# Kernel tuning notes

Hardware: AMD Instinct MI355X
Metric: run time of the kernel (lower is better)

## Reference

```python
import jax, jax.numpy as jnp
import numpy as np

N = 100000
E = 1600000
F_IN = 256
H1, C1 = 4, 32          # layer 1: heads=4, out_channels=32, concat=True -> 128
H2, C2 = 1, 16          # layer 2: heads=1, out_channels=nclass=16, concat=False
SLOPE = 0.2             # leaky relu negative slope


def setup_inputs() -> dict:
    key = jax.random.key(0)
    ks = jax.random.split(key, 10)
    x = jax.random.normal(ks[0], (N, F_IN), dtype=jnp.float32)
    row = jax.random.randint(ks[1], (E,), 0, N, dtype=jnp.int32)      # source j
    off = jax.random.randint(ks[2], (E,), 1, N, dtype=jnp.int32)
    col = ((row + off) % N).astype(jnp.int32)                          # target i, no self loops
    edge_index = jnp.stack([row, col])

    def glorot(k, shape, fan_in, fan_out):
        lim = np.sqrt(6.0 / (fan_in + fan_out))
        return jax.random.uniform(k, shape, jnp.float32, -lim, lim)

    W1 = glorot(ks[3], (F_IN, H1 * C1), F_IN, H1 * C1)
    att1 = glorot(ks[4], (1, H1, 2 * C1), H1, 2 * C1)
    b1 = jnp.zeros((H1 * C1,), jnp.float32)
    W2 = glorot(ks[5], (H1 * C1, H2 * C2), H1 * C1, H2 * C2)
    att2 = glorot(ks[6], (1, H2, 2 * C2), H2, 2 * C2)
    b2 = jnp.zeros((C2,), jnp.float32)
    return {"x": x, "edge_index": edge_index, "W1": W1, "att1": att1,
            "b1": b1, "W2": W2, "att2": att2, "b2": b2}


def gcn_norm(edge_index, num_nodes):
    # add_remaining_self_loops + symmetric normalization (GeoLayer.norm)
    loop = jnp.arange(num_nodes, dtype=edge_index.dtype)
    row = jnp.concatenate([edge_index[0], loop])
    col = jnp.concatenate([edge_index[1], loop])
    w = jnp.ones(row.shape[0], jnp.float32)
    deg = jax.ops.segment_sum(w, row, num_segments=num_nodes)
    dinv = jnp.where(deg > 0, jax.lax.rsqrt(deg), 0.0)
    return row, col, dinv[row] * w * dinv[col]


def segment_softmax(alpha, seg, num_segments):
    amax = jax.ops.segment_max(alpha, seg, num_segments=num_segments)
    ex = jnp.exp(alpha - amax[seg])
    denom = jax.ops.segment_sum(ex, seg, num_segments=num_segments)
    return ex / (denom[seg] + 1e-16)


def geo_layer(x, row, col, ew, W, att, b, heads, out_ch, concat):
    n = x.shape[0]
    xt = (x @ W).reshape(n, heads, out_ch)
    x_i = xt[col]                         # [E+N, H, C] target features
    x_j = xt[row]                         # [E+N, H, C] source features
    wl, wr = att[:, :, :out_ch], att[:, :, out_ch:]
    # (cat([x_i,x_j],-1) * att).sum(-1) == (x_i*wl).sum + (x_j*wr).sum
    alpha = (x_i * wl).sum(-1) + (x_j * wr).sum(-1)     # [E+N, H]
    alpha = jnp.where(alpha >= 0, alpha, SLOPE * alpha)  # leaky_relu
    alpha = segment_softmax(alpha, col, n)
    msg = ew[:, None, None] * x_j * alpha[:, :, None]    # [E+N, H, C]
    out = jax.ops.segment_sum(msg, col, num_segments=n)  # scatter-add to targets
    out = out.reshape(n, heads * out_ch) if concat else out.mean(axis=1)
    return out + b


def reference(x, edge_index, W1, att1, b1, W2, att2, b2):
    # norm is identical for both layers (edge_weight=None each time)
    row, col, ew = gcn_norm(edge_index, x.shape[0])
    h = geo_layer(x, row, col, ew, W1, att1, b1, H1, C1, True)
    h = jax.nn.relu(h)
    out = geo_layer(h, row, col, ew, W2, att2, b2, H2, C2, False)
    return out
```

## Files before the change

### kernel.cpp

```cpp
#include <hip/hip_runtime.h>
#include <math.h>

#define TPB 256
#define SEGN 512
#define SCAP 14336
#define CHB 8192
#define CAPC 12288

__device__ __forceinline__ float lrelu(float a){ return a >= 0.f ? a : 0.2f*a; }

typedef __attribute__((ext_vector_type(8))) short bf16x8;
typedef __attribute__((ext_vector_type(4))) float f32x4;

__device__ __forceinline__ unsigned short bfr(float f){
  unsigned u = __float_as_uint(f);
  return (unsigned short)((u + 0x7fffu + ((u >> 16) & 1u)) >> 16);
}

__device__ __forceinline__ void gl_lds16(const void* g, void* l){
  __builtin_amdgcn_global_load_lds(
      (const __attribute__((address_space(1))) void*)g,
      (__attribute__((address_space(3))) void*)l, 16, 0, 0);
}


__global__ void k_binit(int* __restrict__ bcurC, int* __restrict__ bcurR, int NSEG2){
  int t = threadIdx.x;
  if(t < NSEG2){ bcurC[t] = t*CAPC; bcurR[t] = t*CAPC; }
}

__global__ __launch_bounds__(256) void k_bucket2(const int* __restrict__ rows, const int* __restrict__ cols,
    int* __restrict__ bcurC, int* __restrict__ bcurR,
    unsigned* __restrict__ ebufC, unsigned short* __restrict__ ebufR, int E, int NSEG2){
  __shared__ int lhist[256];
  __shared__ int lbase[256];
  int tid = threadIdx.x;
  int e0 = blockIdx.x * CHB;
  #pragma unroll 1
  for(int r=0; r<4; r++){
    lhist[tid] = 0;
    __syncthreads();
    int eb = e0 + r*2048;
    unsigned pk[8]; int sg[8], rk[8];
    #pragma unroll
    for(int i=0;i<8;i++){
      int e = eb + i*256 + tid;
      sg[i] = -1;
      if(e < E){
        int cc = cols[e], rr = rows[e];
        sg[i] = cc >> 9;
        pk[i] = ((unsigned)(cc & (SEGN-1)) << 17) | (unsigned)rr;
        rk[i] = atomicAdd(&lhist[sg[i]], 1);
      }
    }
    __syncthreads();
    if(tid < NSEG2){
      int c = lhist[tid];
      lbase[tid] = c ? atomicAdd(&bcurC[tid], c) : 0;
    }
    __syncthreads();
    #pragma unroll
    for(int i=0;i<8;i++)
      if(sg[i] >= 0){
        int p = lbase[sg[i]] + rk[i];
        if(p < (sg[i]+1)*CAPC) ebufC[p] = pk[i];
      }
    __syncthreads();
  }
  #pragma unroll 1
  for(int r=0; r<4; r++){
    lhist[tid] = 0;
    __syncthreads();
    int eb = e0 + r*2048;
    int sg[8], rk[8]; unsigned short pv[8];
    #pragma unroll
    for(int i=0;i<8;i++){
      int e = eb + i*256 + tid;
      sg[i] = -1;
      if(e < E){
        int rr = rows[e];
        sg[i] = rr >> 9;
        pv[i] = (unsigned short)(rr & (SEGN-1));
        rk[i] = atomicAdd(&lhist[sg[i]], 1);
      }
    }
    __syncthreads();
    if(tid < NSEG2){
      int c = lhist[tid];
      lbase[tid] = c ? atomicAdd(&bcurR[tid], c) : 0;
    }
    __syncthreads();
    #pragma unroll
    for(int i=0;i<8;i++)
      if(sg[i] >= 0){
        int p = lbase[sg[i]] + rk[i];
        if(p < (sg[i]+1)*CAPC) ebufR[p] = pv[i];
      }
    __syncthreads();
  }
}

__global__ __launch_bounds__(256) void k_cntseg(const int* __restrict__ bcurC, const int* __restrict__ bcurR,
    const unsigned* __restrict__ ebufC, const unsigned short* __restrict__ ebufR,
    int* __restrict__ cnt, float* __restrict__ dinv, int N){
  __shared__ int hc[SEGN];
  __shared__ int hr[SEGN];
  int s = blockIdx.x, tid = threadIdx.x;
  int lo = s*SEGN;
  int nn = min(SEGN, N - lo);
  for(int i=tid; i<SEGN; i+=256){ hc[i] = 0; hr[i] = 0; }
  __syncthreads();
  int cb = s*CAPC;
  int cc = min(bcurC[s] - cb, CAPC);
  int rc = min(bcurR[s] - cb, CAPC);
  for(int j=tid; j<cc; j+=256) atomicAdd(&hc[ebufC[cb + j] >> 17], 1);
  for(int j=tid; j<rc; j+=256) atomicAdd(&hr[ebufR[cb + j]], 1);
  __syncthreads();
  for(int i=tid; i<nn; i+=256){
    cnt[lo+i]  = hc[i] + 1;
    dinv[lo+i] = 1.f / sqrtf((float)(hr[i] + 1));
  }
}

__global__ void k_scan_block(const int* __restrict__ cnt, int* __restrict__ bsum, int N){
  __shared__ int sdata[256];
  int base = blockIdx.x*1024 + threadIdx.x*4;
  int s = 0;
  #pragma unroll
  for(int i=0;i<4;i++){ int idx = base+i; if(idx < N) s += cnt[idx]; }
  sdata[threadIdx.x] = s; __syncthreads();
  for(int off=128; off>0; off>>=1){
    if(threadIdx.x < off) sdata[threadIdx.x] += sdata[threadIdx.x+off];
    __syncthreads();
  }
  if(threadIdx.x == 0) bsum[blockIdx.x] = sdata[0];
}

__global__ void k_scan_bsum(int* bsum, int NB){
  __shared__ int s[256];
  int t = threadIdx.x;
  int v = (t < NB) ? bsum[t] : 0;
  s[t] = v; __syncthreads();
  for(int off=1; off<256; off<<=1){
    int add = (t >= off) ? s[t-off] : 0;
    __syncthreads();
    s[t] += add;
    __syncthreads();
  }
  if(t < NB) bsum[t] = s[t] - v;
}

__global__ void k_scan_write(const int* __restrict__ cnt, const int* __restrict__ bsum,
                             int* __restrict__ offs, int N){
  __shared__ int sdata[256];
  int t = threadIdx.x;
  int base = blockIdx.x*1024 + t*4;
  int v[4]; int s = 0;
  #pragma unroll
  for(int i=0;i<4;i++){ int idx = base+i; v[i] = (idx < N) ? cnt[idx] : 0; s += v[i]; }
  sdata[t] = s; __syncthreads();
  int mine = s;
  for(int off=1; off<256; off<<=1){
    int add = (t >= off) ? sdata[t-off] : 0;
    __syncthreads();
    sdata[t] += add;
    __syncthreads();
  }
  int run = sdata[t] - mine + bsum[blockIdx.x];
  #pragma unroll
  for(int i=0;i<4;i++){
    int idx = base+i;
    if(idx < N){
      offs[idx] = run;
      run += v[i];
      if(idx == N-1) offs[N] = run;
    }
  }
}

__global__ __launch_bounds__(256) void k_sortfill(const int* __restrict__ offs,
    const int* __restrict__ bcurC, const unsigned* __restrict__ ebuf,
    int* __restrict__ csr, int N){
  __shared__ int lcur[SEGN];
  __shared__ int lbuf[SCAP];
  int s = blockIdx.x, tid = threadIdx.x;
  int lo = s*SEGN;
  int nn = min(SEGN, N - lo);
  int base = offs[lo];
  int total = offs[lo+nn] - base;
  int eb = s*CAPC;
  int ec = min(bcurC[s] - eb, CAPC);
  if(total <= SCAP){
    for(int li=tid; li<nn; li+=256){
      int o = offs[lo+li] - base;
      lbuf[o]  = lo + li;
      lcur[li] = o + 1;
    }
    __syncthreads();
    for(int j=tid; j<ec; j+=256){
      unsigned pk = ebuf[eb + j];
      int li  = pk >> 17;
      int row = pk & 0x1FFFF;
      int p = atomicAdd(&lcur[li], 1);
      lbuf[p] = row;
    }
    __syncthreads();
    for(int j=tid; j<total; j+=256) csr[base + j] = lbuf[j];
  } else {
    for(int li=tid; li<nn; li+=256){
      int o = offs[lo+li];
      csr[o] = lo + li;
      lcur[li] = o + 1;
    }
    __syncthreads();
    for(int j=tid; j<ec; j+=256){
      unsigned pk = ebuf[eb + j];
      int li  = pk >> 17;
      int row = pk & 0x1FFFF;
      int p = atomicAdd(&lcur[li], 1);
      csr[p] = row;
    }
  }
}


__global__ void k_prepW(const float* __restrict__ W, short* __restrict__ Whi,
                        short* __restrict__ Wlo){
  int idx = blockIdx.x*256 + threadIdx.x;
  int n = idx >> 8, k = idx & 255;
  float f = W[k*128 + n];
  unsigned short h = bfr(f);
  float hf = __uint_as_float(((unsigned)h) << 16);
  Whi[n*256 + k] = (short)h;
  Wlo[n*256 + k] = (short)bfr(f - hf);
}


__global__ __launch_bounds__(256) void k_prepX(const float* __restrict__ x,
    unsigned short* __restrict__ xhi, unsigned short* __restrict__ xlo,
    long long Ntot, long long NtotPad){
  long long i = ((long long)blockIdx.x*256 + threadIdx.x)*8;
  if(i >= NtotPad) return;
  float v[8] = {0.f,0.f,0.f,0.f,0.f,0.f,0.f,0.f};
  if(i < Ntot){
    const float4* x4 = (const float4*)x;
    float4 a = x4[i>>2], b = x4[(i>>2)+1];
    v[0]=a.x; v[1]=a.y; v[2]=a.z; v[3]=a.w;
    v[4]=b.x; v[5]=b.y; v[6]=b.z; v[7]=b.w;
  }
  unsigned hp[4], lp[4];
  #pragma unroll
  for(int j=0;j<4;j++){
    unsigned short h0 = bfr(v[2*j]), h1 = bfr(v[2*j+1]);
    float r0 = v[2*j]   - __uint_as_float(((unsigned)h0)<<16);
    float r1 = v[2*j+1] - __uint_as_float(((unsigned)h1)<<16);
    hp[j] = (unsigned)h0 | ((unsigned)h1<<16);
    lp[j] = (unsigned)bfr(r0) | ((unsigned)bfr(r1)<<16);
  }
  *((uint4*)(xhi + i)) = make_uint4(hp[0],hp[1],hp[2],hp[3]);
  *((uint4*)(xlo + i)) = make_uint4(lp[0],lp[1],lp[2],lp[3]);
}


#define BUFB 24576
__global__ __launch_bounds__(256) void k_gemm1(
    const unsigned short* __restrict__ xhi, const unsigned short* __restrict__ xlo,
    const short* __restrict__ Whi, const short* __restrict__ Wlo,
    const float* __restrict__ att1,
    unsigned* __restrict__ xtb, float* __restrict__ sl, float* __restrict__ sr, int N){
  __shared__ __align__(16) char smem[2*BUFB];
  float* fx = (float*)smem;
  float* att_sh = (float*)(smem + 17408);

  int tid = threadIdx.x;
  int n0 = blockIdx.x * 64;
  int w = tid >> 6, l = tid & 63;
  int wm = w & 1, wn = w >> 1;
  int lm = l & 15, lq = l >> 4;

  f32x4 acc[2][4];
  #pragma unroll
  for(int a=0;a<2;a++)
    #pragma unroll
    for(int b=0;b<4;b++) acc[a][b] = (f32x4){0.f,0.f,0.f,0.f};

  int ua = (w<<6) | l;
  int ar = ua >> 2, aq = ua & 3;
  int as_ = aq ^ ((ar >> 1) & 3);
  const unsigned short* gAh = xhi + (size_t)(n0 + ar)*256 + as_*8;
  const unsigned short* gAl = xlo + (size_t)(n0 + ar)*256 + as_*8;
  int ub0 = (w<<6) | l,  ub1 = 256 + ub0;
  int br0 = ub0 >> 2, bs0 = (ub0 & 3) ^ ((br0 >> 1) & 3);
  int br1 = ub1 >> 2, bs1 = (ub1 & 3) ^ ((br1 >> 1) & 3);
  const short* gBh0 = Whi + br0*256 + bs0*8;
  const short* gBh1 = Whi + br1*256 + bs1*8;
  const short* gBl0 = Wlo + br0*256 + bs0*8;
  const short* gBl1 = Wlo + br1*256 + bs1*8;
  int woff = w << 10;

  int offA[2], offB[4];
  #pragma unroll
  for(int mt=0;mt<2;mt++){
    int rr = wm*32 + mt*16 + lm;
    offA[mt] = rr*32 + ((lq ^ ((rr>>1)&3)) << 3);
  }
  #pragma unroll
  for(int nt=0;nt<4;nt++){
    int rr = wn*64 + nt*16 + lm;
    offB[nt] = rr*32 + ((lq ^ ((rr>>1)&3)) << 3);
  }

  {
    char* base = smem;
    gl_lds16(gAh,  base          + woff);
    gl_lds16(gAl,  base + 4096   + woff);
    gl_lds16(gBh0, base + 8192   + woff);
    gl_lds16(gBh1, base + 12288  + woff);
    gl_lds16(gBl0, base + 16384  + woff);
    gl_lds16(gBl1, base + 20480  + woff);
  }
  __syncthreads();

  int cur = 0;
  #pragma unroll 1
  for(int c=0;c<8;c++){
    if(c < 7){
      int kb = (c+1) << 5;
      char* base = smem + (cur^1)*BUFB;
      gl_lds16(gAh  + kb, base          + woff);
      gl_lds16(gAl  + kb, base + 4096   + woff);
      gl_lds16(gBh0 + kb, base + 8192   + woff);
      gl_lds16(gBh1 + kb, base + 12288  + woff);
      gl_lds16(gBl0 + kb, base + 16384  + woff);
      gl_lds16(gBl1 + kb, base + 20480  + woff);
    }
    short* Ah = (short*)(smem + cur*BUFB);
    short* Al = (short*)(smem + cur*BUFB + 4096);
    short* Bh = (short*)(smem + cur*BUFB + 8192);
    short* Bl = (short*)(smem + cur*BUFB + 16384);
    bf16x8 ah[2], al2[2];
    #pragma unroll
    for(int mt=0;mt<2;mt++){
      ah[mt]  = *((bf16x8*)&Ah[offA[mt]]);
      al2[mt] = *((bf16x8*)&Al[offA[mt]]);
    }
    #pragma unroll
    for(int nt=0;nt<4;nt++){
      bf16x8 bh = *((bf16x8*)&Bh[offB[nt]]);
      bf16x8 bl = *((bf16x8*)&Bl[offB[nt]]);
      #pragma unroll
      for(int mt=0;mt<2;mt++){
        acc[mt][nt] = __builtin_amdgcn_mfma_f32_16x16x32_bf16(ah[mt],  bh, acc[mt][nt], 0,0,0);
        acc[mt][nt] = __builtin_amdgcn_mfma_f32_16x16x32_bf16(ah[mt],  bl, acc[mt][nt], 0,0,0);
        acc[mt][nt] = __builtin_amdgcn_mfma_f32_16x16x32_bf16(al2[mt], bh, acc[mt][nt], 0,0,0);
      }
    }
    __syncthreads();
    cur ^= 1;
  }

  #pragma unroll
  for(int mt=0;mt<2;mt++){
    #pragma unroll
    for(int v=0;v<4;v++){
      int row = n0 + wm*32 + mt*16 + lq*4 + v;
      if(row < N){
        unsigned p0 = (unsigned)bfr(acc[mt][0][v]) | ((unsigned)bfr(acc[mt][2][v])<<16);
        unsigned p1 = (unsigned)bfr(acc[mt][1][v]) | ((unsigned)bfr(acc[mt][3][v])<<16);
        int jb = wn*32 + lm;
        xtb[(size_t)row*64 + jb]      = p0;
        xtb[(size_t)row*64 + jb + 16] = p1;
      }
    }
  }

  att_sh[tid] = att1[tid];
  #pragma unroll 1
  for(int p=0;p<2;p++){
    __syncthreads();
    if(wn == p){
      #pragma unroll
      for(int mt=0;mt<2;mt++)
        #pragma unroll
        for(int nt=0;nt<4;nt++)
          #pragma unroll
          for(int v=0;v<4;v++)
            fx[(wm*32 + mt*16 + lq*4 + v)*68 + nt*16 + lm] = acc[mt][nt][v];
    }
    __syncthreads();
    if(tid < 128){
      int rloc = tid >> 1, hh = tid & 1;
      int head = p*2 + hh;
      float a = 0.f, b = 0.f;
      #pragma unroll
      for(int c4=0;c4<8;c4++){
        float4 xv  = *((const float4*)&fx[rloc*68 + hh*32 + c4*4]);
        float4 alv = *((const float4*)&att_sh[head*64 + c4*4]);
        float4 arv = *((const float4*)&att_sh[head*64 + 32 + c4*4]);
        a += xv.x*alv.x + xv.y*alv.y + xv.z*alv.z + xv.w*alv.w;
        b += xv.x*arv.x + xv.y*arv.y + xv.z*arv.z + xv.w*arv.w;
      }
      int row = n0 + rloc;
      if(row < N){
        sl[(size_t)row*4 + head] = a;
        sr[(size_t)row*4 + head] = b;
      }
    }
  }
}


__global__ __launch_bounds__(64) void k_agg1(const int* __restrict__ offs, const int* __restrict__ srcs,
    const float* __restrict__ sl, const float* __restrict__ sr, const float* __restrict__ dinv,
    const unsigned* __restrict__ xtb, const float* __restrict__ b1, float* __restrict__ h, int N){
  __shared__ int   s_sh[64];
  __shared__ float w_sh[64*4];
  int n = blockIdx.x;
  if(n >= N) return;
  int lane = threadIdx.x;
  int beg = offs[n], end = offs[n+1];
  int deg = end - beg;
  float4 sln = *((const float4*)(sl + (size_t)n*4));
  int h0 = lane >> 5;
  float den0=0.f,den1=0.f,den2=0.f,den3=0.f;
  float acc0=0.f, acc1=0.f;

  if(deg <= 64){
    int j = beg + lane;
    int s = 0; float wd = 0.f;
    float a0=-1e30f, a1=-1e30f, a2=-1e30f, a3=-1e30f;
    if(j < end){
      s = srcs[j];
      float4 a = *((const float4*)(sr + (size_t)s*4));
      a0 = lrelu(sln.x + a.x);
      a1 = lrelu(sln.y + a.y);
      a2 = lrelu(sln.z + a.z);
      a3 = lrelu(sln.w + a.w);
      wd = dinv[s];
    }
    float m0=a0,m1=a1,m2=a2,m3=a3;
    #pragma unroll
    for(int o=32;o>0;o>>=1){
      m0 = fmaxf(m0, __shfl_xor(m0,o));
      m1 = fmaxf(m1, __shfl_xor(m1,o));
      m2 = fmaxf(m2, __shfl_xor(m2,o));
      m3 = fmaxf(m3, __shfl_xor(m3,o));
    }
    den0 = __expf(a0 - m0);
    den1 = __expf(a1 - m1);
    den2 = __expf(a2 - m2);
    den3 = __expf(a3 - m3);
    s_sh[lane] = s;
    w_sh[lane*4+0] = wd*den0;
    w_sh[lane*4+1] = wd*den1;
    w_sh[lane*4+2] = wd*den2;
    w_sh[lane*4+3] = wd*den3;
    __syncthreads();
    int k = 0;
    for(; k+8<=deg; k+=8){
      int sk[8];
      #pragma unroll
      for(int u=0;u<8;u++) sk[u] = __builtin_amdgcn_readfirstlane(s_sh[k+u]);
      unsigned pv[8];
      #pragma unroll
      for(int u=0;u<8;u++) pv[u] = xtb[(size_t)sk[u]*64 + lane];
      #pragma unroll
      for(int u=0;u<8;u++){
        float2 wv = *((const float2*)&w_sh[(k+u)*4 + h0*2]);
        acc0 += wv.x * __uint_as_float(pv[u] << 16);
        acc1 += wv.y * __uint_as_float(pv[u] & 0xffff0000u);
      }
    }
    for(; k<deg; k++){
      int sk = __builtin_amdgcn_readfirstlane(s_sh[k]);
      unsigned pvv = xtb[(size_t)sk*64 + lane];
      float2 wv = *((const float2*)&w_sh[k*4 + h0*2]);
      acc0 += wv.x * __uint_as_float(pvv << 16);
      acc1 += wv.y * __uint_as_float(pvv & 0xffff0000u);
    }
  } else {
    float m0=-1e30f,m1=-1e30f,m2=-1e30f,m3=-1e30f;
    for(int j=beg+lane; j<end; j+=64){
      int s = srcs[j];
      float4 a = *((const float4*)(sr + (size_t)s*4));
      m0 = fmaxf(m0, lrelu(sln.x + a.x));
      m1 = fmaxf(m1, lrelu(sln.y + a.y));
      m2 = fmaxf(m2, lrelu(sln.z + a.z));
      m3 = fmaxf(m3, lrelu(sln.w + a.w));
    }
    #pragma unroll
    for(int o=32;o>0;o>>=1){
      m0 = fmaxf(m0, __shfl_xor(m0,o));
      m1 = fmaxf(m1, __shfl_xor(m1,o));
      m2 = fmaxf(m2, __shfl_xor(m2,o));
      m3 = fmaxf(m3, __shfl_xor(m3,o));
    }
    for(int c0=beg; c0<end; c0+=64){
      int cnt = min(64, end-c0);
      int j = c0 + lane;
      float e0=0.f,e1=0.f,e2=0.f,e3=0.f, wd=0.f; int s=0;
      if(j<end){
        s = srcs[j];
        float4 a = *((const float4*)(sr + (size_t)s*4));
        e0 = __expf(lrelu(sln.x + a.x) - m0);
        e1 = __expf(lrelu(sln.y + a.y) - m1);
        e2 = __expf(lrelu(sln.z + a.z) - m2);
        e3 = __expf(lrelu(sln.w + a.w) - m3);
        wd = dinv[s];
      }
      den0+=e0; den1+=e1; den2+=e2; den3+=e3;
      s_sh[lane] = s;
      w_sh[lane*4+0] = wd*e0;
      w_sh[lane*4+1] = wd*e1;
      w_sh[lane*4+2] = wd*e2;
      w_sh[lane*4+3] = wd*e3;
      __syncthreads();
      int k = 0;
      for(; k+8<=cnt; k+=8){
        int sk[8];
        #pragma unroll
        for(int u=0;u<8;u++) sk[u] = __builtin_amdgcn_readfirstlane(s_sh[k+u]);
        unsigned pv[8];
        #pragma unroll
        for(int u=0;u<8;u++) pv[u] = xtb[(size_t)sk[u]*64 + lane];
        #pragma unroll
        for(int u=0;u<8;u++){
          float2 wv = *((const float2*)&w_sh[(k+u)*4 + h0*2]);
          acc0 += wv.x * __uint_as_float(pv[u] << 16);
          acc1 += wv.y * __uint_as_float(pv[u] & 0xffff0000u);
        }
      }
      for(; k<cnt; k++){
        int sk = __builtin_amdgcn_readfirstlane(s_sh[k]);
        unsigned pvv = xtb[(size_t)sk*64 + lane];
        float2 wv = *((const float2*)&w_sh[k*4 + h0*2]);
        acc0 += wv.x * __uint_as_float(pvv << 16);
        acc1 += wv.y * __uint_as_float(pvv & 0xffff0000u);
      }
      __syncthreads();
    }
  }
  #pragma unroll
  for(int o=32;o>0;o>>=1){
    den0 += __shfl_xor(den0,o);
    den1 += __shfl_xor(den1,o);
    den2 += __shfl_xor(den2,o);
    den3 += __shfl_xor(den3,o);
  }
  float din = dinv[n];
  int ch0 = (lane < 32) ? lane : lane + 32;
  int ch1 = ch0 + 32;
  float d0 = (lane < 32) ? den0 : den2;
  float d1 = (lane < 32) ? den1 : den3;
  float o0 = din*acc0/(d0 + 1e-16f) + b1[ch0];
  float o1 = din*acc1/(d1 + 1e-16f) + b1[ch1];
  h[(size_t)n*128 + ch0] = o0 > 0.f ? o0 : 0.f;
  h[(size_t)n*128 + ch1] = o1 > 0.f ? o1 : 0.f;
}


__global__ __launch_bounds__(256) void k_gemm2(const float* __restrict__ hmat, const float* __restrict__ W2,
    const float* __restrict__ att2, unsigned* __restrict__ xt2b,
    float* __restrict__ sl2, float* __restrict__ sr2, int N){
  __shared__ float hs[16*132];
  __shared__ float ws[16*132];
  __shared__ float xs[16*16];
  int t = threadIdx.x;
  int n0 = blockIdx.x * 16;
  #pragma unroll
  for(int i=0;i<8;i++){
    int idx = t + 256*i;
    int k = idx >> 4, c = idx & 15;
    ws[c*132 + k] = W2[idx];
  }
  #pragma unroll
  for(int i=0;i<2;i++){
    int idx = t + 256*i;
    int r = idx >> 5, k4 = idx & 31;
    int n = n0 + r;
    float4 v = make_float4(0.f,0.f,0.f,0.f);
    if(n < N) v = ((const float4*)hmat)[(size_t)n*32 + k4];
    *((float4*)&hs[r*132 + k4*4]) = v;
  }
  __syncthreads();
  int r = t >> 4, c = t & 15;
  float acc = 0.f;
  for(int k=0;k<128;k+=4){
    float4 hv = *((const float4*)&hs[r*132+k]);
    float4 wv = *((const float4*)&ws[c*132+k]);
    acc += hv.x*wv.x + hv.y*wv.y + hv.z*wv.z + hv.w*wv.w;
  }
  xs[r*16 + c] = acc;
  __syncthreads();
  int n = n0 + r;
  if(c < 8 && n < N){
    unsigned pk = (unsigned)bfr(xs[r*16+c]) | ((unsigned)bfr(xs[r*16+c+8])<<16);
    xt2b[(size_t)n*8 + c] = pk;
  }
  if(t < 16){
    int nn = n0 + t;
    if(nn < N){
      float a = 0.f, b = 0.f;
      #pragma unroll
      for(int cc=0;cc<16;cc++){ float v = xs[t*16+cc]; a += v*att2[cc]; b += v*att2[16+cc]; }
      sl2[nn] = a; sr2[nn] = b;
    }
  }
}


__global__ __launch_bounds__(64) void k_agg2(const int* __restrict__ offs, const int* __restrict__ srcs,
    const float* __restrict__ sl2, const float* __restrict__ sr2, const float* __restrict__ dinv,
    const unsigned* __restrict__ xt2b, const float* __restrict__ b2, float* __restrict__ out, int N){
  __shared__ int   s_sh[64];
  __shared__ float w_sh[64];
  int n = blockIdx.x;
  if(n >= N) return;
  int lane = threadIdx.x;
  int beg = offs[n], end = offs[n+1];
  int deg = end - beg;
  float sln = sl2[n];
  float den = 0.f, acc0 = 0.f, acc1 = 0.f;
  int grp = lane >> 3, ch = lane & 7;

  if(deg <= 64){
    int j = beg + lane;
    int s = 0; float wd = 0.f; float a = -1e30f;
    if(j < end){
      s = srcs[j];
      a = lrelu(sln + sr2[s]);
      wd = dinv[s];
    }
    float m = a;
    #pragma unroll
    for(int o=32;o>0;o>>=1) m = fmaxf(m, __shfl_xor(m,o));
    float e = __expf(a - m);
    den = e;
    s_sh[lane] = s;
    w_sh[lane] = wd*e;
    __syncthreads();
    for(int k=0;k<deg;k+=8){
      int kk = k + grp;
      if(kk < deg){
        int sk = s_sh[kk];
        float wk = w_sh[kk];
        unsigned pv = xt2b[(size_t)sk*8 + ch];
        acc0 += wk * __uint_as_float(pv << 16);
        acc1 += wk * __uint_as_float(pv & 0xffff0000u);
      }
    }
  } else {
    float m = -1e30f;
    for(int j=beg+lane; j<end; j+=64)
      m = fmaxf(m, lrelu(sln + sr2[srcs[j]]));
    #pragma unroll
    for(int o=32;o>0;o>>=1) m = fmaxf(m, __shfl_xor(m,o));
    for(int c0=beg; c0<end; c0+=64){
      int cnt = min(64, end-c0);
      int j = c0 + lane;
      float e=0.f, wd=0.f; int s=0;
      if(j<end){
        s = srcs[j];
        e = __expf(lrelu(sln + sr2[s]) - m);
        wd = dinv[s];
      }
      den += e;
      s_sh[lane] = s;
      w_sh[lane] = wd*e;
      __syncthreads();
      for(int k=0;k<cnt;k+=8){
        int kk = k + grp;
        if(kk < cnt){
          int sk = s_sh[kk];
          float wk = w_sh[kk];
          unsigned pv = xt2b[(size_t)sk*8 + ch];
          acc0 += wk * __uint_as_float(pv << 16);
          acc1 += wk * __uint_as_float(pv & 0xffff0000u);
        }
      }
      __syncthreads();
    }
  }
  #pragma unroll
  for(int o=32;o>0;o>>=1) den += __shfl_xor(den,o);
  acc0 += __shfl_xor(acc0,8);  acc0 += __shfl_xor(acc0,16);  acc0 += __shfl_xor(acc0,32);
  acc1 += __shfl_xor(acc1,8);  acc1 += __shfl_xor(acc1,16);  acc1 += __shfl_xor(acc1,32);
  if(lane < 8){
    float din = dinv[n];
    out[(size_t)n*16 + lane]     = din*acc0/(den + 1e-16f) + b2[lane];
    out[(size_t)n*16 + lane + 8] = din*acc1/(den + 1e-16f) + b2[lane+8];
  }
}


extern "C" void kernel_launch(void* const* d_in, const int* in_sizes, int n_in,
                              void* d_out, int out_size, void* d_ws, size_t ws_size,
                              hipStream_t stream){
  const float* x    = (const float*)d_in[0];
  const int*   ei   = (const int*)d_in[1];
  const float* W1   = (const float*)d_in[2];
  const float* att1 = (const float*)d_in[3];
  const float* b1   = (const float*)d_in[4];
  const float* W2   = (const float*)d_in[5];
  const float* att2 = (const float*)d_in[6];
  const float* b2   = (const float*)d_in[7];
  int N = in_sizes[0] / 256;
  int E = in_sizes[1] / 2;
  const int* rows = ei;
  const int* cols = ei + E;
  float* out = (float*)d_out;

  int ET    = E + N;
  int Npad  = (N + 63) & ~63;
  int NSEG2 = (N + SEGN - 1) / SEGN;

  char* p = (char*)d_ws;
  auto alloc = [&](size_t bytes)->void*{ void* q = p; p += (bytes + 255) & ~(size_t)255; return q; };
  int*      cnt     = (int*)alloc((size_t)N*4);
  int*      offs    = (int*)alloc((size_t)(N+1)*4);
  int*      bsum    = (int*)alloc(256*4);
  int*      bcurC   = (int*)alloc(256*4);
  int*      bcurR   = (int*)alloc(256*4);
  int*      csr     = (int*)alloc((size_t)ET*4);
  float*    dinv    = (float*)alloc((size_t)N*4);
  unsigned* xtb     = (unsigned*)alloc((size_t)N*64*4);
  float*    sl1     = (float*)alloc((size_t)N*16);
  float*    sr1     = (float*)alloc((size_t)N*16);
  float*    hbuf    = (float*)alloc((size_t)Npad*512);
  unsigned* xt2b    = (unsigned*)alloc((size_t)N*8*4);
  float*    sl2     = (float*)alloc((size_t)N*4);
  float*    sr2     = (float*)alloc((size_t)N*4);
  short*    Whi     = (short*)alloc((size_t)128*256*2);
  short*    Wlo     = (short*)alloc((size_t)128*256*2);
  unsigned short* xhi = (unsigned short*)alloc((size_t)Npad*256*2);

  unsigned*       ebufC = (unsigned*)xtb;
  unsigned short* ebufR = (unsigned short*)(ebufC + (size_t)NSEG2*CAPC);
  unsigned short* xlo   = (unsigned short*)hbuf;

  int NB = (N + 1023) / 1024;
  int gB = (E + CHB - 1) / CHB;

  k_binit<<<1, 256, 0, stream>>>(bcurC, bcurR, NSEG2);
  k_bucket2<<<gB, 256, 0, stream>>>(rows, cols, bcurC, bcurR, ebufC, ebufR, E, NSEG2);
  k_cntseg<<<NSEG2, 256, 0, stream>>>(bcurC, bcurR, ebufC, ebufR, cnt, dinv, N);
  k_scan_block<<<NB, 256, 0, stream>>>(cnt, bsum, N);
  k_scan_bsum<<<1, 256, 0, stream>>>(bsum, NB);
  k_scan_write<<<NB, 256, 0, stream>>>(cnt, bsum, offs, N);
  k_sortfill<<<NSEG2, 256, 0, stream>>>(offs, bcurC, ebufC, csr, N);

  k_prepW<<<128, 256, 0, stream>>>(W1, Whi, Wlo);
  long long Ntot = (long long)N*256, NtotPad = (long long)Npad*256;
  k_prepX<<<(int)((NtotPad + 2047)/2048), 256, 0, stream>>>(x, xhi, xlo, Ntot, NtotPad);
  k_gemm1<<<(N + 63)/64, 256, 0, stream>>>(xhi, xlo, Whi, Wlo, att1, xtb, sl1, sr1, N);
  k_agg1<<<N, 64, 0, stream>>>(offs, csr, sl1, sr1, dinv, xtb, b1, hbuf, N);

  k_gemm2<<<(N + 15)/16, 256, 0, stream>>>(hbuf, W2, att2, xt2b, sl2, sr2, N);
  k_agg2<<<N, 64, 0, stream>>>(offs, csr, sl2, sr2, dinv, xt2b, b2, out, N);
}
```

Measured before the change: 447.4 us.

## Fuse bf16 split of x into GEMM1 and merge scan stages into count kernel

```diff
diff --git a/kernel.cpp b/kernel.cpp
--- a/kernel.cpp
+++ b/kernel.cpp
@@ -23,11 +23,6 @@
       (__attribute__((address_space(3))) void*)l, 16, 0, 0);
 }
 
-
-__global__ void k_binit(int* __restrict__ bcurC, int* __restrict__ bcurR, int NSEG2){
-  int t = threadIdx.x;
-  if(t < NSEG2){ bcurC[t] = t*CAPC; bcurR[t] = t*CAPC; }
-}
 
 __global__ __launch_bounds__(256) void k_bucket2(const int* __restrict__ rows, const int* __restrict__ cols,
     int* __restrict__ bcurC, int* __restrict__ bcurR,
@@ -63,7 +58,7 @@
     for(int i=0;i<8;i++)
       if(sg[i] >= 0){
         int p = lbase[sg[i]] + rk[i];
-        if(p < (sg[i]+1)*CAPC) ebufC[p] = pk[i];
+        if(p < CAPC) ebufC[sg[i]*CAPC + p] = pk[i];
       }
     __syncthreads();
   }
@@ -94,7 +89,7 @@
     for(int i=0;i<8;i++)
       if(sg[i] >= 0){
         int p = lbase[sg[i]] + rk[i];
-        if(p < (sg[i]+1)*CAPC) ebufR[p] = pv[i];
+        if(p < CAPC) ebufR[sg[i]*CAPC + p] = pv[i];
       }
     __syncthreads();
   }
@@ -102,38 +97,34 @@
 
 __global__ __launch_bounds__(256) void k_cntseg(const int* __restrict__ bcurC, const int* __restrict__ bcurR,
     const unsigned* __restrict__ ebufC, const unsigned short* __restrict__ ebufR,
-    int* __restrict__ cnt, float* __restrict__ dinv, int N){
+    int* __restrict__ cnt, float* __restrict__ dinv, int* __restrict__ bsum, int N){
   __shared__ int hc[SEGN];
   __shared__ int hr[SEGN];
+  __shared__ int red[256];
   int s = blockIdx.x, tid = threadIdx.x;
   int lo = s*SEGN;
   int nn = min(SEGN, N - lo);
   for(int i=tid; i<SEGN; i+=256){ hc[i] = 0; hr[i] = 0; }
   __syncthreads();
   int cb = s*CAPC;
-  int cc = min(bcurC[s] - cb, CAPC);
-  int rc = min(bcurR[s] - cb, CAPC);
+  int cc = min(bcurC[s], CAPC);
+  int rc = min(bcurR[s], CAPC);
   for(int j=tid; j<cc; j+=256) atomicAdd(&hc[ebufC[cb + j] >> 17], 1);
   for(int j=tid; j<rc; j+=256) atomicAdd(&hr[ebufR[cb + j]], 1);
   __syncthreads();
+  int tsum = 0;
   for(int i=tid; i<nn; i+=256){
-    cnt[lo+i]  = hc[i] + 1;
+    int c = hc[i] + 1;
+    cnt[lo+i]  = c;
+    tsum += c;
     dinv[lo+i] = 1.f / sqrtf((float)(hr[i] + 1));
   }
-}
-
-__global__ void k_scan_block(const int* __restrict__ cnt, int* __restrict__ bsum, int N){
-  __shared__ int sdata[256];
-  int base = blockIdx.x*1024 + threadIdx.x*4;
-  int s = 0;
-  #pragma unroll
-  for(int i=0;i<4;i++){ int idx = base+i; if(idx < N) s += cnt[idx]; }
-  sdata[threadIdx.x] = s; __syncthreads();
+  red[tid] = tsum; __syncthreads();
   for(int off=128; off>0; off>>=1){
-    if(threadIdx.x < off) sdata[threadIdx.x] += sdata[threadIdx.x+off];
-    __syncthreads();
-  }
-  if(threadIdx.x == 0) bsum[blockIdx.x] = sdata[0];
+    if(tid < off) red[tid] += red[tid+off];
+    __syncthreads();
+  }
+  if(tid == 0) bsum[s] = red[0];
 }
 
 __global__ void k_scan_bsum(int* bsum, int NB){
@@ -154,10 +145,10 @@
                              int* __restrict__ offs, int N){
   __shared__ int sdata[256];
   int t = threadIdx.x;
-  int base = blockIdx.x*1024 + t*4;
-  int v[4]; int s = 0;
-  #pragma unroll
-  for(int i=0;i<4;i++){ int idx = base+i; v[i] = (idx < N) ? cnt[idx] : 0; s += v[i]; }
+  int base = blockIdx.x*512 + t*2;
+  int v0 = (base   < N) ? cnt[base]   : 0;
+  int v1 = (base+1 < N) ? cnt[base+1] : 0;
+  int s = v0 + v1;
   sdata[t] = s; __syncthreads();
   int mine = s;
   for(int off=1; off<256; off<<=1){
@@ -167,14 +158,13 @@
     __syncthreads();
   }
   int run = sdata[t] - mine + bsum[blockIdx.x];
-  #pragma unroll
-  for(int i=0;i<4;i++){
-    int idx = base+i;
-    if(idx < N){
-      offs[idx] = run;
-      run += v[i];
-      if(idx == N-1) offs[N] = run;
-    }
+  if(base < N){
+    offs[base] = run; run += v0;
+    if(base == N-1) offs[N] = run;
+  }
+  if(base+1 < N){
+    offs[base+1] = run; run += v1;
+    if(base+1 == N-1) offs[N] = run;
   }
 }
 
@@ -189,7 +179,7 @@
   int base = offs[lo];
   int total = offs[lo+nn] - base;
   int eb = s*CAPC;
-  int ec = min(bcurC[s] - eb, CAPC);
+  int ec = min(bcurC[s], CAPC);
   if(total <= SCAP){
     for(int li=tid; li<nn; li+=256){
       int o = offs[lo+li] - base;
@@ -236,35 +226,9 @@
 }
 
 
-__global__ __launch_bounds__(256) void k_prepX(const float* __restrict__ x,
-    unsigned short* __restrict__ xhi, unsigned short* __restrict__ xlo,
-    long long Ntot, long long NtotPad){
-  long long i = ((long long)blockIdx.x*256 + threadIdx.x)*8;
-  if(i >= NtotPad) return;
-  float v[8] = {0.f,0.f,0.f,0.f,0.f,0.f,0.f,0.f};
-  if(i < Ntot){
-    const float4* x4 = (const float4*)x;
-    float4 a = x4[i>>2], b = x4[(i>>2)+1];
-    v[0]=a.x; v[1]=a.y; v[2]=a.z; v[3]=a.w;
-    v[4]=b.x; v[5]=b.y; v[6]=b.z; v[7]=b.w;
-  }
-  unsigned hp[4], lp[4];
-  #pragma unroll
-  for(int j=0;j<4;j++){
-    unsigned short h0 = bfr(v[2*j]), h1 = bfr(v[2*j+1]);
-    float r0 = v[2*j]   - __uint_as_float(((unsigned)h0)<<16);
-    float r1 = v[2*j+1] - __uint_as_float(((unsigned)h1)<<16);
-    hp[j] = (unsigned)h0 | ((unsigned)h1<<16);
-    lp[j] = (unsigned)bfr(r0) | ((unsigned)bfr(r1)<<16);
-  }
-  *((uint4*)(xhi + i)) = make_uint4(hp[0],hp[1],hp[2],hp[3]);
-  *((uint4*)(xlo + i)) = make_uint4(lp[0],lp[1],lp[2],lp[3]);
-}
-
-
 #define BUFB 24576
 __global__ __launch_bounds__(256) void k_gemm1(
-    const unsigned short* __restrict__ xhi, const unsigned short* __restrict__ xlo,
+    const float* __restrict__ x,
     const short* __restrict__ Whi, const short* __restrict__ Wlo,
     const float* __restrict__ att1,
     unsigned* __restrict__ xtb, float* __restrict__ sl, float* __restrict__ sr, int N){
@@ -284,11 +248,11 @@
     #pragma unroll
     for(int b=0;b<4;b++) acc[a][b] = (f32x4){0.f,0.f,0.f,0.f};
 
-  int ua = (w<<6) | l;
-  int ar = ua >> 2, aq = ua & 3;
-  int as_ = aq ^ ((ar >> 1) & 3);
-  const unsigned short* gAh = xhi + (size_t)(n0 + ar)*256 + as_*8;
-  const unsigned short* gAl = xlo + (size_t)(n0 + ar)*256 + as_*8;
+  int ua0 = (w<<6) | l, ua1 = 256 + ua0;
+  int ar0 = ua0 >> 3, as0 = (ua0 & 7) ^ (ar0 & 7);
+  int ar1 = ua1 >> 3, as1 = (ua1 & 7) ^ (ar1 & 7);
+  const float* gA0 = x + (size_t)min(n0 + ar0, N-1)*256 + as0*4;
+  const float* gA1 = x + (size_t)min(n0 + ar1, N-1)*256 + as1*4;
   int ub0 = (w<<6) | l,  ub1 = 256 + ub0;
   int br0 = ub0 >> 2, bs0 = (ub0 & 3) ^ ((br0 >> 1) & 3);
   int br1 = ub1 >> 2, bs1 = (ub1 & 3) ^ ((br1 >> 1) & 3);
@@ -298,11 +262,12 @@
   const short* gBl1 = Wlo + br1*256 + bs1*8;
   int woff = w << 10;
 
-  int offA[2], offB[4];
+  int offAf[2][2], offB[4];
   #pragma unroll
   for(int mt=0;mt<2;mt++){
     int rr = wm*32 + mt*16 + lm;
-    offA[mt] = rr*32 + ((lq ^ ((rr>>1)&3)) << 3);
+    offAf[mt][0] = rr*32 + (((2*lq+0) ^ (rr&7)) << 2);
+    offAf[mt][1] = rr*32 + (((2*lq+1) ^ (rr&7)) << 2);
   }
   #pragma unroll
   for(int nt=0;nt<4;nt++){
@@ -312,8 +277,8 @@
 
   {
     char* base = smem;
-    gl_lds16(gAh,  base          + woff);
-    gl_lds16(gAl,  base + 4096   + woff);
+    gl_lds16(gA0,  base          + woff);
+    gl_lds16(gA1,  base + 4096   + woff);
     gl_lds16(gBh0, base + 8192   + woff);
     gl_lds16(gBh1, base + 12288  + woff);
     gl_lds16(gBl0, base + 16384  + woff);
@@ -325,24 +290,31 @@
   #pragma unroll 1
   for(int c=0;c<8;c++){
     if(c < 7){
-      int kb = (c+1) << 5;
+      int kf = (c+1) << 5;
       char* base = smem + (cur^1)*BUFB;
-      gl_lds16(gAh  + kb, base          + woff);
-      gl_lds16(gAl  + kb, base + 4096   + woff);
-      gl_lds16(gBh0 + kb, base + 8192   + woff);
-      gl_lds16(gBh1 + kb, base + 12288  + woff);
-      gl_lds16(gBl0 + kb, base + 16384  + woff);
-      gl_lds16(gBl1 + kb, base + 20480  + woff);
-    }
-    short* Ah = (short*)(smem + cur*BUFB);
-    short* Al = (short*)(smem + cur*BUFB + 4096);
-    short* Bh = (short*)(smem + cur*BUFB + 8192);
-    short* Bl = (short*)(smem + cur*BUFB + 16384);
+      gl_lds16(gA0  + kf, base          + woff);
+      gl_lds16(gA1  + kf, base + 4096   + woff);
+      gl_lds16(gBh0 + kf, base + 8192   + woff);
+      gl_lds16(gBh1 + kf, base + 12288  + woff);
+      gl_lds16(gBl0 + kf, base + 16384  + woff);
+      gl_lds16(gBl1 + kf, base + 20480  + woff);
+    }
+    float* Axf = (float*)(smem + cur*BUFB);
+    short* Bh  = (short*)(smem + cur*BUFB + 8192);
+    short* Bl  = (short*)(smem + cur*BUFB + 16384);
     bf16x8 ah[2], al2[2];
     #pragma unroll
     for(int mt=0;mt<2;mt++){
-      ah[mt]  = *((bf16x8*)&Ah[offA[mt]]);
-      al2[mt] = *((bf16x8*)&Al[offA[mt]]);
+      float4 f0 = *((const float4*)&Axf[offAf[mt][0]]);
+      float4 f1 = *((const float4*)&Axf[offAf[mt][1]]);
+      float fa[8] = {f0.x,f0.y,f0.z,f0.w,f1.x,f1.y,f1.z,f1.w};
+      #pragma unroll
+      for(int j=0;j<8;j++){
+        unsigned short hb = bfr(fa[j]);
+        float hf = __uint_as_float(((unsigned)hb) << 16);
+        ah[mt][j]  = (short)hb;
+        al2[mt][j] = (short)bfr(fa[j] - hf);
+      }
     }
     #pragma unroll
     for(int nt=0;nt<4;nt++){
@@ -711,7 +683,6 @@
   float* out = (float*)d_out;
 
   int ET    = E + N;
-  int Npad  = (N + 63) & ~63;
   int NSEG2 = (N + SEGN - 1) / SEGN;
 
   char* p = (char*)d_ws;
@@ -719,40 +690,36 @@
   int*      cnt     = (int*)alloc((size_t)N*4);
   int*      offs    = (int*)alloc((size_t)(N+1)*4);
   int*      bsum    = (int*)alloc(256*4);
-  int*      bcurC   = (int*)alloc(256*4);
-  int*      bcurR   = (int*)alloc(256*4);
+  int*      bcur    = (int*)alloc(512*4);
   int*      csr     = (int*)alloc((size_t)ET*4);
   float*    dinv    = (float*)alloc((size_t)N*4);
   unsigned* xtb     = (unsigned*)alloc((size_t)N*64*4);
   float*    sl1     = (float*)alloc((size_t)N*16);
   float*    sr1     = (float*)alloc((size_t)N*16);
-  float*    hbuf    = (float*)alloc((size_t)Npad*512);
+  float*    hbuf    = (float*)alloc((size_t)N*128*4);
   unsigned* xt2b    = (unsigned*)alloc((size_t)N*8*4);
   float*    sl2     = (float*)alloc((size_t)N*4);
   float*    sr2     = (float*)alloc((size_t)N*4);
   short*    Whi     = (short*)alloc((size_t)128*256*2);
   short*    Wlo     = (short*)alloc((size_t)128*256*2);
-  unsigned short* xhi = (unsigned short*)alloc((size_t)Npad*256*2);
+
+  int* bcurC = bcur;
+  int* bcurR = bcur + 256;
 
   unsigned*       ebufC = (unsigned*)xtb;
   unsigned short* ebufR = (unsigned short*)(ebufC + (size_t)NSEG2*CAPC);
-  unsigned short* xlo   = (unsigned short*)hbuf;
-
-  int NB = (N + 1023) / 1024;
+
   int gB = (E + CHB - 1) / CHB;
 
-  k_binit<<<1, 256, 0, stream>>>(bcurC, bcurR, NSEG2);
+  hipMemsetAsync(bcur, 0, 512*4, stream);
   k_bucket2<<<gB, 256, 0, stream>>>(rows, cols, bcurC, bcurR, ebufC, ebufR, E, NSEG2);
-  k_cntseg<<<NSEG2, 256, 0, stream>>>(bcurC, bcurR, ebufC, ebufR, cnt, dinv, N);
-  k_scan_block<<<NB, 256, 0, stream>>>(cnt, bsum, N);
-  k_scan_bsum<<<1, 256, 0, stream>>>(bsum, NB);
-  k_scan_write<<<NB, 256, 0, stream>>>(cnt, bsum, offs, N);
+  k_cntseg<<<NSEG2, 256, 0, stream>>>(bcurC, bcurR, ebufC, ebufR, cnt, dinv, bsum, N);
+  k_scan_bsum<<<1, 256, 0, stream>>>(bsum, NSEG2);
+  k_scan_write<<<NSEG2, 256, 0, stream>>>(cnt, bsum, offs, N);
   k_sortfill<<<NSEG2, 256, 0, stream>>>(offs, bcurC, ebufC, csr, N);
 
   k_prepW<<<128, 256, 0, stream>>>(W1, Whi, Wlo);
-  long long Ntot = (long long)N*256, NtotPad = (long long)Npad*256;
-  k_prepX<<<(int)((NtotPad + 2047)/2048), 256, 0, stream>>>(x, xhi, xlo, Ntot, NtotPad);
-  k_gemm1<<<(N + 63)/64, 256, 0, stream>>>(xhi, xlo, Whi, Wlo, att1, xtb, sl1, sr1, N);
+  k_gemm1<<<(N + 63)/64, 256, 0, stream>>>(x, Whi, Wlo, att1, xtb, sl1, sr1, N);
   k_agg1<<<N, 64, 0, stream>>>(offs, csr, sl1, sr1, dinv, xtb, b1, hbuf, N);
 
   k_gemm2<<<(N + 15)/16, 256, 0, stream>>>(hbuf, W2, att2, xt2b, sl2, sr2, N);
```

Result: faster. 414.7 us (-7.3%).
